# Kernel optimization log

Measured on AMD Instinct MI355X. Metric: run time of the kernel, lower is better.

Reference implementation:

```python
import jax, jax.numpy as jnp
import numpy as np

N_NODES = 10000
N_EDGES = 640000
IN_FEAT = 128
HIDDEN = 128
CLASSES = 2
NEG_SLOPE = 0.2


def glorot(key, shape):
    lim = float(np.sqrt(6.0 / (shape[0] + shape[-1])))
    return jax.random.uniform(key, shape, jnp.float32, -lim, lim)


def setup_inputs() -> dict:
    key = jax.random.key(0)
    ks = jax.random.split(key, 10)
    x = jax.random.normal(ks[0], (N_NODES, IN_FEAT), jnp.float32)
    edge_index = jax.random.randint(ks[1], (2, N_EDGES), 0, N_NODES, jnp.int64)
    return {
        "x": x,
        "edge_index": edge_index,
        "W1": glorot(ks[2], (IN_FEAT, HIDDEN)),
        "a_src1": glorot(ks[3], (HIDDEN, 1))[:, 0],
        "a_dst1": glorot(ks[4], (HIDDEN, 1))[:, 0],
        "b1": jnp.zeros((HIDDEN,), jnp.float32),
        "W2": glorot(ks[5], (HIDDEN, CLASSES)),
        "a_src2": glorot(ks[6], (CLASSES, 1))[:, 0],
        "a_dst2": glorot(ks[7], (CLASSES, 1))[:, 0],
        "b2": jnp.zeros((CLASSES,), jnp.float32),
    }


def gat_conv(x, src, dst, W, a_src, a_dst, b, n_nodes):
    # x: [N, Fin] -> h: [N, Fout]
    h = x @ W
    # per-node attention logits (single head)
    alpha_s = h @ a_src  # [N]
    alpha_d = h @ a_dst  # [N]
    e = jax.nn.leaky_relu(alpha_s[src] + alpha_d[dst], NEG_SLOPE)  # [E]
    # segment softmax over incoming edges of each dst node
    m = jax.ops.segment_max(e, dst, num_segments=n_nodes)
    ex = jnp.exp(e - m[dst])
    denom = jax.ops.segment_sum(ex, dst, num_segments=n_nodes)
    w = ex / denom[dst]  # [E]
    # weighted scatter-aggregate of source messages
    out = jax.ops.segment_sum(h[src] * w[:, None], dst, num_segments=n_nodes)
    return out + b


def reference(x, edge_index, W1, a_src1, a_dst1, b1, W2, a_src2, a_dst2, b2):
    n = x.shape[0]
    # PyG GATConv default: add self-loops
    loops = jnp.arange(n, dtype=edge_index.dtype)
    src = jnp.concatenate([edge_index[0], loops])
    dst = jnp.concatenate([edge_index[1], loops])
    h = gat_conv(x, src, dst, W1, a_src1, a_dst1, b1, n)
    h = jax.nn.relu(h)
    out = gat_conv(h, src, dst, W2, a_src2, a_dst2, b2, n)
    return out
```

## Files before the change

### kernel.cpp

```cpp
#include <hip/hip_runtime.h>
#include <hip/hip_bf16.h>

#define NN 10000
#define NE 640000
#define ETOT (NE + NN)
#define FEAT 128
#define NEG 0.2f
#define CAP 160
#define NBUCK 157
#define BCAP 5120
#define EPB 4096
#define NB1 ((ETOT + EPB - 1) / EPB)
#define GEMM_ROWS 16
#define NBG (NN / GEMM_ROWS)
#define NJOB1 (NB1 + NBG)
#define NJAGG ((NN + 3) / 4)

typedef short bf16x8 __attribute__((ext_vector_type(8)));
typedef float f32x4  __attribute__((ext_vector_type(4)));

__device__ __forceinline__ short f2bf(float f) {
    unsigned u = __float_as_uint(f);
    unsigned r = (u + 0x7FFFu + ((u >> 16) & 1u)) >> 16;
    return (short)r;
}

union ShMem {
    struct {
        int hist[160]; int scan[256]; int excl[160]; int cursor[160]; int base[160];
        unsigned int pairs[EPB];
    } p;
    struct { float rs[GEMM_ROWS][2]; float rd[GEMM_ROWS][2]; } g;
};

__device__ __forceinline__ int detect64(const void* ep) {
    const unsigned long long* p64 = (const unsigned long long*)ep;
    unsigned long long v = p64[threadIdx.x & 63];
    unsigned long long bal = __ballot((v >> 32) != 0ULL);
    return (bal == 0ULL) ? 1 : 0;
}

__global__ __launch_bounds__(256) void prep_kernel(
        const float* __restrict__ W1, const float* __restrict__ a_src1,
        const float* __restrict__ a_dst1,
        unsigned short* __restrict__ W1t, float* __restrict__ wa, float* __restrict__ wd,
        int* __restrict__ gbcnt) {
    int idx = blockIdx.x * 256 + threadIdx.x;
    if (idx < FEAT * FEAT) {
        int n = idx >> 7, k = idx & 127;
        W1t[n * FEAT + k] = (unsigned short)f2bf(W1[k * FEAT + n]);
    }
    int i2 = idx - FEAT * FEAT;
    if (i2 >= 0 && i2 < NBUCK * 16) gbcnt[i2] = 0;
    int i3 = idx - (FEAT * FEAT + NBUCK * 16);
    if (i3 >= 0 && i3 < FEAT) {
        float s = 0.f;
        for (int k = 0; k < FEAT; k++) s += W1[i3 * FEAT + k] * a_src1[k];
        wa[i3] = s;
    } else if (i3 >= FEAT && i3 < 2 * FEAT) {
        int j = i3 - FEAT;
        float s = 0.f;
        for (int k = 0; k < FEAT; k++) s += W1[j * FEAT + k] * a_dst1[k];
        wd[j] = s;
    }
}

__device__ __forceinline__ void bin_job(const void* ep, int flag64,
        int* __restrict__ gbcnt, unsigned int* __restrict__ staged,
        ShMem& sh, int tid, int job) {
    for (int i = tid; i < 160; i += 256) sh.p.hist[i] = 0;
    __syncthreads();
    const int e0 = job * EPB;
    int nE = ETOT - e0; if (nE > EPB) nE = EPB;
    const bool full = (nE == EPB);
    unsigned int key[16];
    if (full) {
#pragma unroll
        for (int k = 0; k < 16; k++) {
            int e = e0 + tid + k * 256, s, d;
            if (e < NE) {
                if (flag64) { const long long* p = (const long long*)ep; s = (int)p[e]; d = (int)p[NE + e]; }
                else        { const int* p = (const int*)ep;       s = p[e];       d = p[NE + e]; }
            } else { s = e - NE; d = s; }
            key[k] = ((unsigned)d << 14) | (unsigned)s;
            atomicAdd(&sh.p.hist[d >> 6], 1);
        }
    } else {
        for (int k = 0; k < 16; k++) {
            int idx = tid + k * 256;
            if (idx < nE) {
                int e = e0 + idx, s, d;
                if (e < NE) {
                    if (flag64) { const long long* p = (const long long*)ep; s = (int)p[e]; d = (int)p[NE + e]; }
                    else        { const int* p = (const int*)ep;       s = p[e];       d = p[NE + e]; }
                } else { s = e - NE; d = s; }
                atomicAdd(&sh.p.hist[d >> 6], 1);
            }
        }
    }
    __syncthreads();
    sh.p.scan[tid] = (tid < 160) ? sh.p.hist[tid] : 0;
    __syncthreads();
    for (int off = 1; off < 256; off <<= 1) {
        int t = (tid >= off) ? sh.p.scan[tid - off] : 0;
        __syncthreads();
        sh.p.scan[tid] += t;
        __syncthreads();
    }
    if (tid < 160) {
        int ex = sh.p.scan[tid] - sh.p.hist[tid];
        sh.p.excl[tid] = ex;
        sh.p.cursor[tid] = ex;
        sh.p.base[tid] = (tid < NBUCK && sh.p.hist[tid] > 0)
                           ? atomicAdd(&gbcnt[tid * 16], sh.p.hist[tid]) : 0;
    }
    __syncthreads();
    if (full) {
#pragma unroll
        for (int k = 0; k < 16; k++) {
            int b = key[k] >> 20;
            int pos = atomicAdd(&sh.p.cursor[b], 1);
            sh.p.pairs[pos] = key[k];
        }
    } else {
        for (int k = 0; k < 16; k++) {
            int idx = tid + k * 256;
            if (idx < nE) {
                int e = e0 + idx, s, d;
                if (e < NE) {
                    if (flag64) { const long long* p = (const long long*)ep; s = (int)p[e]; d = (int)p[NE + e]; }
                    else        { const int* p = (const int*)ep;       s = p[e];       d = p[NE + e]; }
                } else { s = e - NE; d = s; }
                unsigned int kk = ((unsigned)d << 14) | (unsigned)s;
                int pos = atomicAdd(&sh.p.cursor[d >> 6], 1);
                sh.p.pairs[pos] = kk;
            }
        }
    }
    __syncthreads();
    for (int i = tid; i < nE; i += 256) {
        unsigned int kk = sh.p.pairs[i];
        int b = kk >> 20;
        int idx = sh.p.base[b] + (i - sh.p.excl[b]);
        if (idx < BCAP) staged[b * BCAP + idx] = kk;
    }
}

__device__ __forceinline__ void gemm_job(
        const float* __restrict__ x, const unsigned short* __restrict__ W1t,
        const float* __restrict__ wa, const float* __restrict__ wd,
        unsigned short* __restrict__ h1, float* __restrict__ as1, float* __restrict__ ad1,
        ShMem& sh, int tid, int gb) {
    const int row0 = gb * GEMM_ROWS;
    const int j = tid & 127, half = tid >> 7;
    const int lane = tid & 63, wv = tid >> 6;

    float wav = wa[j], wdv = wd[j];
    int wpair = wv & 1;
    for (int rr = 0; rr < 8; rr++) {
        int r = half * 8 + rr;
        float xv = x[(size_t)(row0 + r) * FEAT + j];
        float vs = xv * wav, vd = xv * wdv;
#pragma unroll
        for (int o = 32; o; o >>= 1) { vs += __shfl_xor(vs, o); vd += __shfl_xor(vd, o); }
        if (lane == 0) { sh.g.rs[r][wpair] = vs; sh.g.rd[r][wpair] = vd; }
    }

    const int m = lane & 15, g = lane >> 4;
    const int n0 = wv * 32;
    const float* arow = x + (size_t)(row0 + m) * FEAT + g * 8;
    const unsigned short* bb0 = W1t + (size_t)(n0 + m) * FEAT + g * 8;
    const unsigned short* bb1 = W1t + (size_t)(n0 + 16 + m) * FEAT + g * 8;
    f32x4 acc0 = {0.f, 0.f, 0.f, 0.f}, acc1 = {0.f, 0.f, 0.f, 0.f};
#pragma unroll
    for (int kt = 0; kt < 4; kt++) {
        float4 v0 = *(const float4*)(arow + kt * 32);
        float4 v1 = *(const float4*)(arow + kt * 32 + 4);
        bf16x8 a;
        a[0] = f2bf(v0.x); a[1] = f2bf(v0.y); a[2] = f2bf(v0.z); a[3] = f2bf(v0.w);
        a[4] = f2bf(v1.x); a[5] = f2bf(v1.y); a[6] = f2bf(v1.z); a[7] = f2bf(v1.w);
        bf16x8 b0 = *(const bf16x8*)(bb0 + kt * 32);
        bf16x8 b1 = *(const bf16x8*)(bb1 + kt * 32);
        acc0 = __builtin_amdgcn_mfma_f32_16x16x32_bf16(a, b0, acc0, 0, 0, 0);
        acc1 = __builtin_amdgcn_mfma_f32_16x16x32_bf16(a, b1, acc1, 0, 0, 0);
    }
#pragma unroll
    for (int r = 0; r < 4; r++) {
        int row = row0 + g * 4 + r;
        h1[(size_t)row * FEAT + n0 + m]      = (unsigned short)f2bf(acc0[r]);
        h1[(size_t)row * FEAT + n0 + 16 + m] = (unsigned short)f2bf(acc1[r]);
    }
    __syncthreads();
    if (tid < GEMM_ROWS) {
        int row = row0 + tid;
        as1[row] = sh.g.rs[tid][0] + sh.g.rs[tid][1];
        ad1[row] = sh.g.rd[tid][0] + sh.g.rd[tid][1];
    }
}

__global__ __launch_bounds__(256) void fat1_kernel(const void* ep,
        const float* __restrict__ x, const unsigned short* __restrict__ W1t,
        const float* __restrict__ wa, const float* __restrict__ wd,
        int* __restrict__ gbcnt, unsigned int* __restrict__ staged,
        unsigned short* __restrict__ h1, float* __restrict__ as1, float* __restrict__ ad1) {
    __shared__ ShMem sh;
    int blk = blockIdx.x, tid = threadIdx.x;
    if (blk < NB1) { int f = detect64(ep); bin_job(ep, f, gbcnt, staged, sh, tid, blk); }
    else gemm_job(x, W1t, wa, wd, h1, as1, ad1, sh, tid, blk - NB1);
}

__global__ __launch_bounds__(256) void scatter2_kernel(const int* __restrict__ gbcnt,
        const unsigned int* __restrict__ staged, int* __restrict__ slots, int* __restrict__ deg) {
    __shared__ int ncnt[64];
    int b = blockIdx.x, tid = threadIdx.x;
    if (tid < 64) ncnt[tid] = 0;
    __syncthreads();
    int total = gbcnt[b * 16]; if (total > BCAP) total = BCAP;
    for (int i = tid; i < total; i += 256) {
        unsigned int kk = staged[b * BCAP + i];
        int d = kk >> 14, s = kk & 0x3FFF;
        int lp = atomicAdd(&ncnt[d & 63], 1);
        if (lp < CAP) slots[d * CAP + lp] = s;
    }
    __syncthreads();
    if (tid < 64) {
        int node = b * 64 + tid;
        if (node < NN) deg[node] = min(ncnt[tid], CAP);
    }
}

__global__ __launch_bounds__(256) void agg1_kernel(const int* __restrict__ deg,
        const int* __restrict__ slots, const float* __restrict__ as1,
        const float* __restrict__ ad1, const unsigned int* __restrict__ h1u,
        const float* __restrict__ b1, const float* __restrict__ W2,
        const float* __restrict__ a_src2, const float* __restrict__ a_dst2,
        float* __restrict__ h2, float* __restrict__ as2, float* __restrict__ ad2) {
    __shared__ float2 ws_s[4][CAP];
    int tid = threadIdx.x;
    int wi = tid >> 6, lane = tid & 63;
    int v = blockIdx.x * 4 + wi;
    if (v >= NN) return;
    int c = deg[v];
    const int base = v * CAP;
    float adv = ad1[v];

    int i0 = lane, i1 = lane + 64, i2 = lane + 128;
    float dsum = 0.f;
    if (i0 < c) {
        int s = slots[base + i0];
        float t = as1[s] + adv; t = (t > 0.f) ? t : NEG * t;
        float w = __expf(fminf(t, 80.f));
        ws_s[wi][i0] = make_float2(w, __int_as_float(s)); dsum += w;
    }
    if (i1 < c) {
        int s = slots[base + i1];
        float t = as1[s] + adv; t = (t > 0.f) ? t : NEG * t;
        float w = __expf(fminf(t, 80.f));
        ws_s[wi][i1] = make_float2(w, __int_as_float(s)); dsum += w;
    }
    if (i2 < c) {
        int s = slots[base + i2];
        float t = as1[s] + adv; t = (t > 0.f) ? t : NEG * t;
        float w = __expf(fminf(t, 80.f));
        ws_s[wi][i2] = make_float2(w, __int_as_float(s)); dsum += w;
    }
#pragma unroll
    for (int o = 32; o; o >>= 1) dsum += __shfl_xor(dsum, o);

    float ax = 0.f, ay = 0.f;
#pragma unroll 4
    for (int i = 0; i < c; i++) {
        float2 ws = ws_s[wi][i];
        float wgt = ws.x;
        int s = __float_as_int(ws.y);
        unsigned int u = h1u[s * 64 + lane];
        ax += wgt * __uint_as_float(u << 16);
        ay += wgt * __uint_as_float(u & 0xFFFF0000u);
    }
    float inv = 1.f / dsum;
    float2 bb = ((const float2*)b1)[lane];
    float hx = fmaxf(ax * inv + bb.x, 0.f);
    float hy = fmaxf(ay * inv + bb.y, 0.f);

    const float2* w2p = (const float2*)W2;
    float2 wc0 = w2p[2 * lane], wc1 = w2p[2 * lane + 1];
    float c0 = hx * wc0.x + hy * wc1.x;
    float c1 = hx * wc0.y + hy * wc1.y;
#pragma unroll
    for (int o = 32; o; o >>= 1) { c0 += __shfl_down(c0, o); c1 += __shfl_down(c1, o); }
    if (lane == 0) {
        ((float2*)h2)[v] = make_float2(c0, c1);
        as2[v] = c0 * a_src2[0] + c1 * a_src2[1];
        ad2[v] = c0 * a_dst2[0] + c1 * a_dst2[1];
    }
}

__global__ __launch_bounds__(256) void agg2_kernel(const int* __restrict__ deg,
        const int* __restrict__ slots, const float* __restrict__ as2,
        const float* __restrict__ ad2, const float* __restrict__ h2,
        const float* __restrict__ b2, float* __restrict__ out) {
    int tid = threadIdx.x;
    int wi = tid >> 6, lane = tid & 63;
    int v = blockIdx.x * 4 + wi;
    if (v >= NN) return;
    int c = deg[v];
    int base = v * CAP;
    float adv = ad2[v];
    float dsum = 0.f, a0 = 0.f, a1 = 0.f;
    for (int i = lane; i < c; i += 64) {
        int s = slots[base + i];
        float e = as2[s] + adv;
        e = (e > 0.f) ? e : NEG * e;
        float w = __expf(fminf(e, 80.f));
        dsum += w;
        float2 hv = ((const float2*)h2)[s];
        a0 += w * hv.x; a1 += w * hv.y;
    }
#pragma unroll
    for (int o = 32; o; o >>= 1) {
        dsum += __shfl_xor(dsum, o);
        a0 += __shfl_xor(a0, o);
        a1 += __shfl_xor(a1, o);
    }
    if (lane == 0) {
        out[v * 2]     = a0 / dsum + b2[0];
        out[v * 2 + 1] = a1 / dsum + b2[1];
    }
}

extern "C" void kernel_launch(void* const* d_in, const int* in_sizes, int n_in,
                              void* d_out, int out_size, void* d_ws, size_t ws_size,
                              hipStream_t stream) {
    const float* x      = (const float*)d_in[0];
    const void*  edges  = d_in[1];
    const float* W1     = (const float*)d_in[2];
    const float* a_src1 = (const float*)d_in[3];
    const float* a_dst1 = (const float*)d_in[4];
    const float* b1     = (const float*)d_in[5];
    const float* W2     = (const float*)d_in[6];
    const float* a_src2 = (const float*)d_in[7];
    const float* a_dst2 = (const float*)d_in[8];
    const float* b2     = (const float*)d_in[9];
    float* out = (float*)d_out;

    char* w = (char*)d_ws;
    size_t off = 0;
    auto alloc = [&](size_t bytes) { void* p = w + off; off += (bytes + 255) & ~size_t(255); return p; };
    int*             gbcnt  = (int*)alloc((size_t)NBUCK * 16 * 4);
    unsigned int*    staged = (unsigned int*)alloc((size_t)NBUCK * BCAP * 4);
    int*             slots  = (int*)alloc((size_t)NN * CAP * 4);
    int*             deg    = (int*)alloc((size_t)NN * 4);
    unsigned short*  h1     = (unsigned short*)alloc((size_t)NN * FEAT * 2);
    unsigned short*  W1t    = (unsigned short*)alloc((size_t)FEAT * FEAT * 2);
    float*           wa     = (float*)alloc(FEAT * 4);
    float*           wd     = (float*)alloc(FEAT * 4);
    float*           as1    = (float*)alloc(NN * 4);
    float*           ad1    = (float*)alloc(NN * 4);
    float*           h2     = (float*)alloc(NN * 2 * 4);
    float*           as2    = (float*)alloc(NN * 4);
    float*           ad2    = (float*)alloc(NN * 4);

    int prep_items = FEAT * FEAT + NBUCK * 16 + 2 * FEAT;
    prep_kernel<<<(prep_items + 255) / 256, 256, 0, stream>>>(W1, a_src1, a_dst1,
                                                              W1t, wa, wd, gbcnt);
    fat1_kernel<<<NJOB1, 256, 0, stream>>>(edges, x, W1t, wa, wd,
                                           gbcnt, staged, h1, as1, ad1);
    scatter2_kernel<<<NBUCK, 256, 0, stream>>>(gbcnt, staged, slots, deg);
    agg1_kernel<<<NJAGG, 256, 0, stream>>>(deg, slots, as1, ad1,
                                           (const unsigned int*)h1, b1,
                                           W2, a_src2, a_dst2, h2, as2, ad2);
    agg2_kernel<<<NJAGG, 256, 0, stream>>>(deg, slots, as2, ad2, h2, b2, out);
}
```

Measured before the change: 60.50 us.

## Replace global atomic bucket staging with per-job sorted chunks and histogram tables

```diff
diff --git a/kernel.cpp b/kernel.cpp
--- a/kernel.cpp
+++ b/kernel.cpp
@@ -8,9 +8,9 @@
 #define NEG 0.2f
 #define CAP 160
 #define NBUCK 157
-#define BCAP 5120
-#define EPB 4096
+#define EPB 2048
 #define NB1 ((ETOT + EPB - 1) / EPB)
+#define NB1P 320
 #define GEMM_ROWS 16
 #define NBG (NN / GEMM_ROWS)
 #define NJOB1 (NB1 + NBG)
@@ -27,7 +27,7 @@
 
 union ShMem {
     struct {
-        int hist[160]; int scan[256]; int excl[160]; int cursor[160]; int base[160];
+        int hist[160]; int scan[256]; int excl[160]; int cursor[160];
         unsigned int pairs[EPB];
     } p;
     struct { float rs[GEMM_ROWS][2]; float rd[GEMM_ROWS][2]; } g;
@@ -43,16 +43,13 @@
 __global__ __launch_bounds__(256) void prep_kernel(
         const float* __restrict__ W1, const float* __restrict__ a_src1,
         const float* __restrict__ a_dst1,
-        unsigned short* __restrict__ W1t, float* __restrict__ wa, float* __restrict__ wd,
-        int* __restrict__ gbcnt) {
+        unsigned short* __restrict__ W1t, float* __restrict__ wa, float* __restrict__ wd) {
     int idx = blockIdx.x * 256 + threadIdx.x;
     if (idx < FEAT * FEAT) {
         int n = idx >> 7, k = idx & 127;
         W1t[n * FEAT + k] = (unsigned short)f2bf(W1[k * FEAT + n]);
     }
-    int i2 = idx - FEAT * FEAT;
-    if (i2 >= 0 && i2 < NBUCK * 16) gbcnt[i2] = 0;
-    int i3 = idx - (FEAT * FEAT + NBUCK * 16);
+    int i3 = idx - FEAT * FEAT;
     if (i3 >= 0 && i3 < FEAT) {
         float s = 0.f;
         for (int k = 0; k < FEAT; k++) s += W1[i3 * FEAT + k] * a_src1[k];
@@ -66,17 +63,17 @@
 }
 
 __device__ __forceinline__ void bin_job(const void* ep, int flag64,
-        int* __restrict__ gbcnt, unsigned int* __restrict__ staged,
+        unsigned int* __restrict__ jstage, int* __restrict__ jhist, int* __restrict__ jexcl,
         ShMem& sh, int tid, int job) {
     for (int i = tid; i < 160; i += 256) sh.p.hist[i] = 0;
     __syncthreads();
     const int e0 = job * EPB;
     int nE = ETOT - e0; if (nE > EPB) nE = EPB;
     const bool full = (nE == EPB);
-    unsigned int key[16];
+    unsigned int key[8];
     if (full) {
 #pragma unroll
-        for (int k = 0; k < 16; k++) {
+        for (int k = 0; k < 8; k++) {
             int e = e0 + tid + k * 256, s, d;
             if (e < NE) {
                 if (flag64) { const long long* p = (const long long*)ep; s = (int)p[e]; d = (int)p[NE + e]; }
@@ -86,7 +83,7 @@
             atomicAdd(&sh.p.hist[d >> 6], 1);
         }
     } else {
-        for (int k = 0; k < 16; k++) {
+        for (int k = 0; k < 8; k++) {
             int idx = tid + k * 256;
             if (idx < nE) {
                 int e = e0 + idx, s, d;
@@ -111,19 +108,21 @@
         int ex = sh.p.scan[tid] - sh.p.hist[tid];
         sh.p.excl[tid] = ex;
         sh.p.cursor[tid] = ex;
-        sh.p.base[tid] = (tid < NBUCK && sh.p.hist[tid] > 0)
-                           ? atomicAdd(&gbcnt[tid * 16], sh.p.hist[tid]) : 0;
+        if (tid < NBUCK) {
+            jhist[tid * NB1P + job] = sh.p.hist[tid];
+            jexcl[tid * NB1P + job] = ex;
+        }
     }
     __syncthreads();
     if (full) {
 #pragma unroll
-        for (int k = 0; k < 16; k++) {
+        for (int k = 0; k < 8; k++) {
             int b = key[k] >> 20;
             int pos = atomicAdd(&sh.p.cursor[b], 1);
             sh.p.pairs[pos] = key[k];
         }
     } else {
-        for (int k = 0; k < 16; k++) {
+        for (int k = 0; k < 8; k++) {
             int idx = tid + k * 256;
             if (idx < nE) {
                 int e = e0 + idx, s, d;
@@ -138,12 +137,8 @@
         }
     }
     __syncthreads();
-    for (int i = tid; i < nE; i += 256) {
-        unsigned int kk = sh.p.pairs[i];
-        int b = kk >> 20;
-        int idx = sh.p.base[b] + (i - sh.p.excl[b]);
-        if (idx < BCAP) staged[b * BCAP + idx] = kk;
-    }
+    for (int i = tid; i < nE; i += 256)
+        jstage[job * EPB + i] = sh.p.pairs[i];
 }
 
 __device__ __forceinline__ void gemm_job(
@@ -201,26 +196,38 @@
 __global__ __launch_bounds__(256) void fat1_kernel(const void* ep,
         const float* __restrict__ x, const unsigned short* __restrict__ W1t,
         const float* __restrict__ wa, const float* __restrict__ wd,
-        int* __restrict__ gbcnt, unsigned int* __restrict__ staged,
+        unsigned int* __restrict__ jstage, int* __restrict__ jhist, int* __restrict__ jexcl,
         unsigned short* __restrict__ h1, float* __restrict__ as1, float* __restrict__ ad1) {
     __shared__ ShMem sh;
     int blk = blockIdx.x, tid = threadIdx.x;
-    if (blk < NB1) { int f = detect64(ep); bin_job(ep, f, gbcnt, staged, sh, tid, blk); }
+    if (blk < NB1) { int f = detect64(ep); bin_job(ep, f, jstage, jhist, jexcl, sh, tid, blk); }
     else gemm_job(x, W1t, wa, wd, h1, as1, ad1, sh, tid, blk - NB1);
 }
 
-__global__ __launch_bounds__(256) void scatter2_kernel(const int* __restrict__ gbcnt,
-        const unsigned int* __restrict__ staged, int* __restrict__ slots, int* __restrict__ deg) {
+__global__ __launch_bounds__(256) void scatter2_kernel(
+        const unsigned int* __restrict__ jstage, const int* __restrict__ jhist,
+        const int* __restrict__ jexcl, int* __restrict__ slots, int* __restrict__ deg) {
+    __shared__ int jcnt_s[NB1P];
+    __shared__ int jex_s[NB1P];
     __shared__ int ncnt[64];
     int b = blockIdx.x, tid = threadIdx.x;
     if (tid < 64) ncnt[tid] = 0;
-    __syncthreads();
-    int total = gbcnt[b * 16]; if (total > BCAP) total = BCAP;
-    for (int i = tid; i < total; i += 256) {
-        unsigned int kk = staged[b * BCAP + i];
-        int d = kk >> 14, s = kk & 0x3FFF;
-        int lp = atomicAdd(&ncnt[d & 63], 1);
-        if (lp < CAP) slots[d * CAP + lp] = s;
+    for (int j = tid; j < NB1; j += 256) {
+        jcnt_s[j] = jhist[b * NB1P + j];
+        jex_s[j]  = jexcl[b * NB1P + j];
+    }
+    __syncthreads();
+    int wv = tid >> 6, lane = tid & 63;
+    for (int j = wv; j < NB1; j += 4) {
+        int cnt = jcnt_s[j];
+        if (cnt == 0) continue;
+        const unsigned int* src = jstage + (size_t)j * EPB + jex_s[j];
+        for (int i = lane; i < cnt; i += 64) {
+            unsigned int kk = src[i];
+            int d = kk >> 14, s = kk & 0x3FFF;
+            int lp = atomicAdd(&ncnt[d & 63], 1);
+            if (lp < CAP) slots[d * CAP + lp] = s;
+        }
     }
     __syncthreads();
     if (tid < 64) {
@@ -346,8 +353,9 @@
     char* w = (char*)d_ws;
     size_t off = 0;
     auto alloc = [&](size_t bytes) { void* p = w + off; off += (bytes + 255) & ~size_t(255); return p; };
-    int*             gbcnt  = (int*)alloc((size_t)NBUCK * 16 * 4);
-    unsigned int*    staged = (unsigned int*)alloc((size_t)NBUCK * BCAP * 4);
+    unsigned int*    jstage = (unsigned int*)alloc((size_t)NB1 * EPB * 4);
+    int*             jhist  = (int*)alloc((size_t)NBUCK * NB1P * 4);
+    int*             jexcl  = (int*)alloc((size_t)NBUCK * NB1P * 4);
     int*             slots  = (int*)alloc((size_t)NN * CAP * 4);
     int*             deg    = (int*)alloc((size_t)NN * 4);
     unsigned short*  h1     = (unsigned short*)alloc((size_t)NN * FEAT * 2);
@@ -360,12 +368,12 @@
     float*           as2    = (float*)alloc(NN * 4);
     float*           ad2    = (float*)alloc(NN * 4);
 
-    int prep_items = FEAT * FEAT + NBUCK * 16 + 2 * FEAT;
+    int prep_items = FEAT * FEAT + 2 * FEAT;
     prep_kernel<<<(prep_items + 255) / 256, 256, 0, stream>>>(W1, a_src1, a_dst1,
-                                                              W1t, wa, wd, gbcnt);
+                                                              W1t, wa, wd);
     fat1_kernel<<<NJOB1, 256, 0, stream>>>(edges, x, W1t, wa, wd,
-                                           gbcnt, staged, h1, as1, ad1);
-    scatter2_kernel<<<NBUCK, 256, 0, stream>>>(gbcnt, staged, slots, deg);
+                                           jstage, jhist, jexcl, h1, as1, ad1);
+    scatter2_kernel<<<NBUCK, 256, 0, stream>>>(jstage, jhist, jexcl, slots, deg);
     agg1_kernel<<<NJAGG, 256, 0, stream>>>(deg, slots, as1, ad1,
                                            (const unsigned int*)h1, b1,
                                            W2, a_src2, a_dst2, h2, as2, ad2);
```

Result: slower. 89.49 us (+47.9%).

## Compute layer-1 attention weights and softmax denominators during edge scatter

Applied to the files above, without the earlier changes.

```diff
diff --git a/kernel.cpp b/kernel.cpp
--- a/kernel.cpp
+++ b/kernel.cpp
@@ -209,29 +209,44 @@
     else gemm_job(x, W1t, wa, wd, h1, as1, ad1, sh, tid, blk - NB1);
 }
 
-__global__ __launch_bounds__(256) void scatter2_kernel(const int* __restrict__ gbcnt,
-        const unsigned int* __restrict__ staged, int* __restrict__ slots, int* __restrict__ deg) {
-    __shared__ int ncnt[64];
+__global__ __launch_bounds__(1024) void scatter2_kernel(const int* __restrict__ gbcnt,
+        const unsigned int* __restrict__ staged, const float* __restrict__ as1,
+        const float* __restrict__ ad1, float2* __restrict__ slots2,
+        int* __restrict__ deg, float* __restrict__ dsum_g) {
+    __shared__ int   ncnt[64];
+    __shared__ float dsum_s[64];
+    __shared__ float adl[64];
     int b = blockIdx.x, tid = threadIdx.x;
-    if (tid < 64) ncnt[tid] = 0;
+    if (tid < 64) {
+        ncnt[tid] = 0; dsum_s[tid] = 0.f;
+        int node = b * 64 + tid;
+        adl[tid] = (node < NN) ? ad1[node] : 0.f;
+    }
     __syncthreads();
     int total = gbcnt[b * 16]; if (total > BCAP) total = BCAP;
-    for (int i = tid; i < total; i += 256) {
+    for (int i = tid; i < total; i += 1024) {
         unsigned int kk = staged[b * BCAP + i];
         int d = kk >> 14, s = kk & 0x3FFF;
+        float t = as1[s] + adl[d & 63];
+        t = (t > 0.f) ? t : NEG * t;
+        float w = __expf(fminf(t, 80.f));
         int lp = atomicAdd(&ncnt[d & 63], 1);
-        if (lp < CAP) slots[d * CAP + lp] = s;
+        atomicAdd(&dsum_s[d & 63], w);
+        if (lp < CAP) slots2[d * CAP + lp] = make_float2(w, __int_as_float(s));
     }
     __syncthreads();
     if (tid < 64) {
         int node = b * 64 + tid;
-        if (node < NN) deg[node] = min(ncnt[tid], CAP);
+        if (node < NN) {
+            deg[node] = min(ncnt[tid], CAP);
+            dsum_g[node] = dsum_s[tid];
+        }
     }
 }
 
 __global__ __launch_bounds__(256) void agg1_kernel(const int* __restrict__ deg,
-        const int* __restrict__ slots, const float* __restrict__ as1,
-        const float* __restrict__ ad1, const unsigned int* __restrict__ h1u,
+        const float2* __restrict__ slots2, const float* __restrict__ dsum_g,
+        const unsigned int* __restrict__ h1u,
         const float* __restrict__ b1, const float* __restrict__ W2,
         const float* __restrict__ a_src2, const float* __restrict__ a_dst2,
         float* __restrict__ h2, float* __restrict__ as2, float* __restrict__ ad2) {
@@ -241,31 +256,12 @@
     int v = blockIdx.x * 4 + wi;
     if (v >= NN) return;
     int c = deg[v];
+    float dsum = dsum_g[v];
     const int base = v * CAP;
-    float adv = ad1[v];
-
-    int i0 = lane, i1 = lane + 64, i2 = lane + 128;
-    float dsum = 0.f;
-    if (i0 < c) {
-        int s = slots[base + i0];
-        float t = as1[s] + adv; t = (t > 0.f) ? t : NEG * t;
-        float w = __expf(fminf(t, 80.f));
-        ws_s[wi][i0] = make_float2(w, __int_as_float(s)); dsum += w;
-    }
-    if (i1 < c) {
-        int s = slots[base + i1];
-        float t = as1[s] + adv; t = (t > 0.f) ? t : NEG * t;
-        float w = __expf(fminf(t, 80.f));
-        ws_s[wi][i1] = make_float2(w, __int_as_float(s)); dsum += w;
-    }
-    if (i2 < c) {
-        int s = slots[base + i2];
-        float t = as1[s] + adv; t = (t > 0.f) ? t : NEG * t;
-        float w = __expf(fminf(t, 80.f));
-        ws_s[wi][i2] = make_float2(w, __int_as_float(s)); dsum += w;
-    }
-#pragma unroll
-    for (int o = 32; o; o >>= 1) dsum += __shfl_xor(dsum, o);
+
+    if (lane < c)       ws_s[wi][lane]       = slots2[base + lane];
+    if (lane + 64 < c)  ws_s[wi][lane + 64]  = slots2[base + lane + 64];
+    if (lane + 128 < c) ws_s[wi][lane + 128] = slots2[base + lane + 128];
 
     float ax = 0.f, ay = 0.f;
 #pragma unroll 4
@@ -296,7 +292,7 @@
 }
 
 __global__ __launch_bounds__(256) void agg2_kernel(const int* __restrict__ deg,
-        const int* __restrict__ slots, const float* __restrict__ as2,
+        const float2* __restrict__ slots2, const float* __restrict__ as2,
         const float* __restrict__ ad2, const float* __restrict__ h2,
         const float* __restrict__ b2, float* __restrict__ out) {
     int tid = threadIdx.x;
@@ -308,7 +304,7 @@
     float adv = ad2[v];
     float dsum = 0.f, a0 = 0.f, a1 = 0.f;
     for (int i = lane; i < c; i += 64) {
-        int s = slots[base + i];
+        int s = __float_as_int(slots2[base + i].y);
         float e = as2[s] + adv;
         e = (e > 0.f) ? e : NEG * e;
         float w = __expf(fminf(e, 80.f));
@@ -348,8 +344,9 @@
     auto alloc = [&](size_t bytes) { void* p = w + off; off += (bytes + 255) & ~size_t(255); return p; };
     int*             gbcnt  = (int*)alloc((size_t)NBUCK * 16 * 4);
     unsigned int*    staged = (unsigned int*)alloc((size_t)NBUCK * BCAP * 4);
-    int*             slots  = (int*)alloc((size_t)NN * CAP * 4);
+    float2*          slots2 = (float2*)alloc((size_t)NN * CAP * 8);
     int*             deg    = (int*)alloc((size_t)NN * 4);
+    float*           dsum_g = (float*)alloc((size_t)NN * 4);
     unsigned short*  h1     = (unsigned short*)alloc((size_t)NN * FEAT * 2);
     unsigned short*  W1t    = (unsigned short*)alloc((size_t)FEAT * FEAT * 2);
     float*           wa     = (float*)alloc(FEAT * 4);
@@ -365,9 +362,10 @@
                                                               W1t, wa, wd, gbcnt);
     fat1_kernel<<<NJOB1, 256, 0, stream>>>(edges, x, W1t, wa, wd,
                                            gbcnt, staged, h1, as1, ad1);
-    scatter2_kernel<<<NBUCK, 256, 0, stream>>>(gbcnt, staged, slots, deg);
-    agg1_kernel<<<NJAGG, 256, 0, stream>>>(deg, slots, as1, ad1,
+    scatter2_kernel<<<NBUCK, 1024, 0, stream>>>(gbcnt, staged, as1, ad1,
+                                                slots2, deg, dsum_g);
+    agg1_kernel<<<NJAGG, 256, 0, stream>>>(deg, slots2, dsum_g,
                                            (const unsigned int*)h1, b1,
                                            W2, a_src2, a_dst2, h2, as2, ad2);
-    agg2_kernel<<<NJAGG, 256, 0, stream>>>(deg, slots, as2, ad2, h2, b2, out);
-}
+    agg2_kernel<<<NJAGG, 256, 0, stream>>>(deg, slots2, as2, ad2, h2, b2, out);
+}
```

Result: no change. 60.98 us (+0.8%).
